# Kernel tuning notes

Measured on AMD Instinct MI355X. Metric: run time of the kernel, lower is better.

Reference implementation:

```python
import jax, jax.numpy as jnp
import numpy as np

N, F_IN, E0, C = 4096, 512, 12288, 16
E = E0 + N  # after self loops
HID1, HID2 = 32, 16
LPA_ITERS = 5


def setup_inputs() -> dict:
    key = jax.random.key(0)
    ks = jax.random.split(key, 16)
    def glorot(k, shp):
        lim = float(np.sqrt(6.0 / (shp[0] + shp[1])))
        return jax.random.uniform(k, shp, jnp.float32, -lim, lim)
    return {
        "x": jax.random.normal(ks[0], (N, F_IN), jnp.float32),
        "edge_index": jax.random.randint(ks[1], (2, E0), 0, N, jnp.int64),
        "y": jax.random.randint(ks[2], (N,), 0, C, jnp.int64),
        "train_mask": jax.random.bernoulli(ks[3], 0.5, (N,)),
        "W_edge": glorot(ks[4], (E, E)),
        "b_edge": jnp.zeros((E,), jnp.float32),
        "W1": glorot(ks[5], (F_IN, HID1)), "b1": jnp.zeros((HID1,), jnp.float32),
        "W2": glorot(ks[6], (HID1, HID2)), "b2": jnp.zeros((HID2,), jnp.float32),
        "W3": glorot(ks[7], (HID2, HID2)), "b3": jnp.zeros((HID2,), jnp.float32),
        "W4": glorot(ks[8], (HID2, C)), "b4": jnp.zeros((C,), jnp.float32),
    }


def reference(x, edge_index, y, train_mask, W_edge, b_edge, W1, b1, W2, b2, W3, b3, W4, b4):
    n = x.shape[0]
    # add self loops
    loops = jnp.tile(jnp.arange(n, dtype=edge_index.dtype)[None, :], (2, 1))
    ei = jnp.concatenate([edge_index, loops], axis=1)  # [2, E]
    row, col = ei[0], ei[1]
    # edge_weight = Linear(ones(E))
    ew = jnp.ones((ei.shape[1],), x.dtype) @ W_edge.T + b_edge  # [E]
    # degree normalization (faithful: deg[row] * ew, inf masked to 0)
    deg = jax.ops.segment_sum(ew, col, num_segments=n)
    deg = jnp.where(jnp.isinf(deg), 0.0, deg)
    ew = deg[row] * ew

    def gcn(h, W, b):
        h = h @ W + b                      # [N, out]
        m = ew[:, None] * h[row]           # gather + scale, [E, out]
        return jax.ops.segment_sum(m, col, num_segments=n)

    h = jax.nn.relu(gcn(x, W1, b1))
    h = jax.nn.relu(gcn(h, W2, b2))
    h = jax.nn.relu(gcn(h, W3, b3))
    h = gcn(h, W4, b4)                     # [N, C]

    # LPA: propagate masked one-hot labels with same edge weights
    yh = jax.nn.one_hot(y, C, dtype=x.dtype) * train_mask[:, None].astype(x.dtype)
    for _ in range(LPA_ITERS):
        yh = jax.ops.segment_sum(ew[:, None] * yh[row], col, num_segments=n)

    return jax.nn.log_softmax(h, axis=1), jax.nn.log_softmax(yh, axis=1)
```

## Files before the change

kernel.cpp:

```cpp
#include <hip/hip_runtime.h>
#include <math.h>

#define N_NODES 4096
#define F_IN    512
#define E0_EDGES 12288
#define E_TOT   16384
#define C_CLS   16
#define HID1    32
#define HID2    16
#define T       256
#define MAXDEG  64
#define DB      512
#define ZB      4
#define RB0     (DB + ZB)

__global__ __launch_bounds__(256) void big_kernel(const float* __restrict__ W_edge,
                                                  const float* __restrict__ b_edge,
                                                  const float* __restrict__ x,
                                                  const float* __restrict__ W1,
                                                  const float* __restrict__ b1,
                                                  float* __restrict__ ew_raw,
                                                  float* __restrict__ bufA,
                                                  int* __restrict__ cnt,
                                                  float* __restrict__ deg) {
    const int b = blockIdx.x, t = threadIdx.x;
    if (b < DB) {
        const int idx = b * T + t;
        const int n = idx >> 5, f = idx & 31;
        const float* xr = x + (size_t)n * F_IN;
        float acc = b1[f];
        #pragma unroll 8
        for (int k = 0; k < F_IN; ++k) acc = fmaf(xr[k], W1[k * HID1 + f], acc);
        bufA[idx] = acc;
    } else if (b < RB0) {
        for (int i = (b - DB) * T + t; i < N_NODES; i += ZB * T) {
            cnt[i] = 0; deg[i] = 0.f;
        }
    } else {
        const int row = b - RB0;
        const float4* p = (const float4*)(W_edge + (size_t)row * E_TOT);
        float s = 0.f;
        #pragma unroll 4
        for (int i = t; i < E_TOT / 4; i += T) {
            float4 v = p[i];
            s += (v.x + v.y) + (v.z + v.w);
        }
        #pragma unroll
        for (int off = 32; off > 0; off >>= 1) s += __shfl_down(s, off, 64);
        __shared__ float sm[4];
        const int lane = t & 63, wave = t >> 6;
        if (lane == 0) sm[wave] = s;
        __syncthreads();
        if (t == 0) ew_raw[row] = (sm[0] + sm[1]) + (sm[2] + sm[3]) + b_edge[row];
    }
}

__global__ __launch_bounds__(256) void fill_kernel(const int* __restrict__ ei,
                                                   const float* __restrict__ ew_raw,
                                                   int* __restrict__ cnt,
                                                   float* __restrict__ deg,
                                                   int* __restrict__ srow,
                                                   float* __restrict__ ewp) {
    const int e = blockIdx.x * T + threadIdx.x;
    const int rowe = (e < E0_EDGES) ? ei[e] : (e - E0_EDGES);
    const int col  = (e < E0_EDGES) ? ei[E0_EDGES + e] : (e - E0_EDGES);
    const float w = ew_raw[e];
    const int slot = atomicAdd(&cnt[col], 1);
    if (slot < MAXDEG) {
        srow[col * MAXDEG + slot] = rowe;
        ewp[col * MAXDEG + slot]  = w;
    }
    atomicAdd(&deg[col], w);
}

__device__ inline void lsm_store(float acc, float* __restrict__ dst, int n, int f) {
    float mx = acc;
    #pragma unroll
    for (int off = 8; off > 0; off >>= 1) mx = fmaxf(mx, __shfl_xor(mx, off, 16));
    float ss = expf(acc - mx);
    #pragma unroll
    for (int off = 8; off > 0; off >>= 1) ss += __shfl_xor(ss, off, 16);
    dst[n * 16 + f] = acc - mx - logf(ss);
}

__global__ __launch_bounds__(256) void phase4_kernel(const float* __restrict__ bufA,
                                                     const int* __restrict__ srow,
                                                     const float* __restrict__ ewp,
                                                     const float* __restrict__ deg,
                                                     const int* __restrict__ cnt,
                                                     const float* __restrict__ W2,
                                                     const float* __restrict__ b2,
                                                     const int* __restrict__ y,
                                                     const int* __restrict__ mask,
                                                     float* __restrict__ bufB,
                                                     float* __restrict__ ew_s,
                                                     float* __restrict__ yhA) {
    const int b = blockIdx.x, t = threadIdx.x;
    if (b < 512) {
        const int nl = t >> 5, f = t & 31;
        const int n = b * 8 + nl;
        const int base = n * MAXDEG;
        const int c = min(cnt[n], MAXDEG);
        float acc = 0.f;
        for (int j = 0; j < c; ++j) {
            const int r = srow[base + j];
            float d = deg[r]; if (isinf(d)) d = 0.f;
            const float w = d * ewp[base + j];
            if (f == 0) ew_s[base + j] = w;
            acc = fmaf(w, bufA[r * HID1 + f], acc);
        }
        acc = fmaxf(acc, 0.f);
        __shared__ float sm[8][HID1];
        sm[nl][f] = acc;
        __syncthreads();
        if (f < 16) {
            float o = b2[f];
            #pragma unroll
            for (int k = 0; k < HID1; ++k) o = fmaf(sm[nl][k], W2[k * 16 + f], o);
            bufB[n * 16 + f] = o;
        }
    } else {
        const int nl = t >> 4, f = t & 15;
        const int n = (b - 512) * 16 + nl;
        const int base = n * MAXDEG;
        const int c = min(cnt[n], MAXDEG);
        float acc = 0.f;
        for (int j = 0; j < c; ++j) {
            const int r = srow[base + j];
            float d = deg[r]; if (isinf(d)) d = 0.f;
            const float w = d * ewp[base + j];
            const float v = (mask[r] != 0 && y[r] == f) ? 1.f : 0.f;
            acc = fmaf(w, v, acc);
        }
        yhA[n * 16 + f] = acc;
    }
}

template <bool HASG, bool DENSE, bool GSOFT, bool LSOFT>
__global__ __launch_bounds__(256) void phase_kernel(const float* __restrict__ srcG,
                                                    const float* __restrict__ W,
                                                    const float* __restrict__ bb,
                                                    float* __restrict__ dstG,
                                                    const float* __restrict__ srcL,
                                                    float* __restrict__ dstL,
                                                    const int* __restrict__ srow,
                                                    const float* __restrict__ ew_s,
                                                    const int* __restrict__ cnt) {
    const int b = blockIdx.x, t = threadIdx.x;
    const int nl = t >> 4, f = t & 15;
    if (HASG && b < 256) {
        const int n = b * 16 + nl;
        const int base = n * MAXDEG;
        const int c = min(cnt[n], MAXDEG);
        float acc = 0.f;
        for (int j = 0; j < c; ++j)
            acc = fmaf(ew_s[base + j], srcG[srow[base + j] * 16 + f], acc);
        if constexpr (DENSE) {
            acc = fmaxf(acc, 0.f);
            __shared__ float sm[16][16];
            sm[nl][f] = acc;
            __syncthreads();
            float o = bb[f];
            #pragma unroll
            for (int k = 0; k < 16; ++k) o = fmaf(sm[nl][k], W[k * 16 + f], o);
            dstG[n * 16 + f] = o;
        } else if constexpr (GSOFT) {
            lsm_store(acc, dstG, n, f);
        }
    } else {
        const int n = (b - (HASG ? 256 : 0)) * 16 + nl;
        const int base = n * MAXDEG;
        const int c = min(cnt[n], MAXDEG);
        float acc = 0.f;
        for (int j = 0; j < c; ++j)
            acc = fmaf(ew_s[base + j], srcL[srow[base + j] * 16 + f], acc);
        if constexpr (LSOFT) lsm_store(acc, dstL, n, f);
        else                 dstL[n * 16 + f] = acc;
    }
}

extern "C" void kernel_launch(void* const* d_in, const int* in_sizes, int n_in,
                              void* d_out, int out_size, void* d_ws, size_t ws_size,
                              hipStream_t stream) {
    const float* x      = (const float*)d_in[0];
    const int*   ei     = (const int*)d_in[1];
    const int*   y      = (const int*)d_in[2];
    const int*   mask   = (const int*)d_in[3];
    const float* W_edge = (const float*)d_in[4];
    const float* b_edge = (const float*)d_in[5];
    const float* W1 = (const float*)d_in[6];  const float* b1 = (const float*)d_in[7];
    const float* W2 = (const float*)d_in[8];  const float* b2 = (const float*)d_in[9];
    const float* W3 = (const float*)d_in[10]; const float* b3 = (const float*)d_in[11];
    const float* W4 = (const float*)d_in[12]; const float* b4 = (const float*)d_in[13];
    float* out = (float*)d_out;

    float* ws     = (float*)d_ws;
    float* ew_raw = ws;
    float* bufA   = ew_raw + E_TOT;
    float* bufB   = bufA + N_NODES * HID1;
    float* yhA    = bufB + N_NODES * C_CLS;
    float* yhB    = yhA + N_NODES * C_CLS;
    float* ewp    = yhB + N_NODES * C_CLS;
    float* ew_s   = ewp + N_NODES * MAXDEG;
    float* deg    = ew_s + N_NODES * MAXDEG;
    int*   cnt    = (int*)(deg + N_NODES);
    int*   srow   = cnt + N_NODES;

    big_kernel<<<RB0 + E_TOT, T, 0, stream>>>(W_edge, b_edge, x, W1, b1,
                                              ew_raw, bufA, cnt, deg);
    fill_kernel<<<E_TOT / T, T, 0, stream>>>(ei, ew_raw, cnt, deg, srow, ewp);

    phase4_kernel<<<768, T, 0, stream>>>(bufA, srow, ewp, deg, cnt, W2, b2,
                                         y, mask, bufB, ew_s, yhA);
    phase_kernel<true, true, false, false><<<512, T, 0, stream>>>(
        bufB, W3, b3, bufA, yhA, yhB, srow, ew_s, cnt);
    phase_kernel<true, true, false, false><<<512, T, 0, stream>>>(
        bufA, W4, b4, bufB, yhB, yhA, srow, ew_s, cnt);
    phase_kernel<true, false, true, false><<<512, T, 0, stream>>>(
        bufB, nullptr, nullptr, out, yhA, yhB, srow, ew_s, cnt);
    phase_kernel<false, false, false, true><<<256, T, 0, stream>>>(
        nullptr, nullptr, nullptr, nullptr, yhB, out + (size_t)N_NODES * C_CLS,
        srow, ew_s, cnt);
}
```

Before: 215.6 us.

## Fuse edge-bucket fill into W_edge row-sum kernel with one wave per row

Each W_edge row sum now runs on a single 64-lane wave instead of a 256-thread block, so four rows share a block and the shared-memory reduction and __syncthreads go away. The lane-0 thread then inserts the edge into its column bucket and adds to the degree directly, which removes the separate fill kernel launch. Zeroing of cnt/deg moves to a small kernel launched beforehand. The atomics are now spread across the long row-sum phase rather than issued as one burst, and the change trades one launch for another.

```diff
diff --git a/kernel.cpp b/kernel.cpp
--- a/kernel.cpp
+++ b/kernel.cpp
@@ -11,18 +11,26 @@
 #define T       256
 #define MAXDEG  64
 #define DB      512
-#define ZB      4
-#define RB0     (DB + ZB)
+#define RWB     (E_TOT / 4)
+
+__global__ __launch_bounds__(256) void zero_kernel(int* __restrict__ cnt,
+                                                   float* __restrict__ deg) {
+    const int i = blockIdx.x * T + threadIdx.x;
+    if (i < N_NODES) { cnt[i] = 0; deg[i] = 0.f; }
+}
 
 __global__ __launch_bounds__(256) void big_kernel(const float* __restrict__ W_edge,
                                                   const float* __restrict__ b_edge,
                                                   const float* __restrict__ x,
                                                   const float* __restrict__ W1,
                                                   const float* __restrict__ b1,
+                                                  const int* __restrict__ ei,
                                                   float* __restrict__ ew_raw,
                                                   float* __restrict__ bufA,
                                                   int* __restrict__ cnt,
-                                                  float* __restrict__ deg) {
+                                                  float* __restrict__ deg,
+                                                  int* __restrict__ srow,
+                                                  float* __restrict__ ewp) {
     const int b = blockIdx.x, t = threadIdx.x;
     if (b < DB) {
         const int idx = b * T + t;
@@ -32,45 +40,30 @@
         #pragma unroll 8
         for (int k = 0; k < F_IN; ++k) acc = fmaf(xr[k], W1[k * HID1 + f], acc);
         bufA[idx] = acc;
-    } else if (b < RB0) {
-        for (int i = (b - DB) * T + t; i < N_NODES; i += ZB * T) {
-            cnt[i] = 0; deg[i] = 0.f;
-        }
     } else {
-        const int row = b - RB0;
-        const float4* p = (const float4*)(W_edge + (size_t)row * E_TOT);
+        const int wave = t >> 6, lane = t & 63;
+        const int e = (b - DB) * 4 + wave;
+        const float4* p = (const float4*)(W_edge + (size_t)e * E_TOT);
         float s = 0.f;
         #pragma unroll 4
-        for (int i = t; i < E_TOT / 4; i += T) {
+        for (int i = lane; i < E_TOT / 4; i += 64) {
             float4 v = p[i];
             s += (v.x + v.y) + (v.z + v.w);
         }
         #pragma unroll
         for (int off = 32; off > 0; off >>= 1) s += __shfl_down(s, off, 64);
-        __shared__ float sm[4];
-        const int lane = t & 63, wave = t >> 6;
-        if (lane == 0) sm[wave] = s;
-        __syncthreads();
-        if (t == 0) ew_raw[row] = (sm[0] + sm[1]) + (sm[2] + sm[3]) + b_edge[row];
+        if (lane == 0) {
+            const float w = s + b_edge[e];
+            ew_raw[e] = w;
+            const int col = (e < E0_EDGES) ? ei[E0_EDGES + e] : (e - E0_EDGES);
+            const int slot = atomicAdd(&cnt[col], 1);
+            if (slot < MAXDEG) {
+                srow[col * MAXDEG + slot] = (e < E0_EDGES) ? ei[e] : (e - E0_EDGES);
+                ewp[col * MAXDEG + slot]  = w;
+            }
+            atomicAdd(&deg[col], w);
+        }
     }
-}
-
-__global__ __launch_bounds__(256) void fill_kernel(const int* __restrict__ ei,
-                                                   const float* __restrict__ ew_raw,
-                                                   int* __restrict__ cnt,
-                                                   float* __restrict__ deg,
-                                                   int* __restrict__ srow,
-                                                   float* __restrict__ ewp) {
-    const int e = blockIdx.x * T + threadIdx.x;
-    const int rowe = (e < E0_EDGES) ? ei[e] : (e - E0_EDGES);
-    const int col  = (e < E0_EDGES) ? ei[E0_EDGES + e] : (e - E0_EDGES);
-    const float w = ew_raw[e];
-    const int slot = atomicAdd(&cnt[col], 1);
-    if (slot < MAXDEG) {
-        srow[col * MAXDEG + slot] = rowe;
-        ewp[col * MAXDEG + slot]  = w;
-    }
-    atomicAdd(&deg[col], w);
 }
 
 __device__ inline void lsm_store(float acc, float* __restrict__ dst, int n, int f) {
@@ -206,9 +199,10 @@
     int*   cnt    = (int*)(deg + N_NODES);
     int*   srow   = cnt + N_NODES;
 
-    big_kernel<<<RB0 + E_TOT, T, 0, stream>>>(W_edge, b_edge, x, W1, b1,
-                                              ew_raw, bufA, cnt, deg);
-    fill_kernel<<<E_TOT / T, T, 0, stream>>>(ei, ew_raw, cnt, deg, srow, ewp);
+    zero_kernel<<<(N_NODES + T - 1) / T, T, 0, stream>>>(cnt, deg);
+
+    big_kernel<<<DB + RWB, T, 0, stream>>>(W_edge, b_edge, x, W1, b1, ei,
+                                           ew_raw, bufA, cnt, deg, srow, ewp);
 
     phase4_kernel<<<768, T, 0, stream>>>(bufA, srow, ewp, deg, cnt, W2, b2,
                                          y, mask, bufB, ew_s, yhA);
```

After: 235.3 us. +9.1%, slower.
